# Optimization experiments

Hardware: AMD Instinct MI355X
Metric: run time of the kernel (lower is better)

## Reference

```python
import jax, jax.numpy as jnp
import numpy as np

H = 16          # num_heads
W = 256         # attention_window
D_MODEL = 1024
D_FF = 4096
EPS = 1e-5


def _layernorm(x, g, b):
    mu = jnp.mean(x, axis=-1, keepdims=True)
    var = jnp.mean(jnp.square(x - mu), axis=-1, keepdims=True)
    return (x - mu) * jax.lax.rsqrt(var + EPS) * g + b


def _sliding_attn(q, k, v, w):
    # q,k,v: [B,H,S,d]; each query attends to keys in [i-w, i+w]
    B, Hh, S, d = q.shape
    nc = S // w
    qc = q.reshape(B, Hh, nc, w, d)
    kp = jnp.pad(k, ((0, 0), (0, 0), (w, w), (0, 0)))
    vp = jnp.pad(v, ((0, 0), (0, 0), (w, w), (0, 0)))
    # gather 3w keys per chunk (prev w, current w, next w)
    idx = (jnp.arange(nc) * w)[:, None] + jnp.arange(3 * w)[None, :]  # [nc, 3w]
    kc = kp[:, :, idx, :]  # [B,H,nc,3w,d]
    vc = vp[:, :, idx, :]
    scores = jnp.einsum('bhcqd,bhckd->bhcqk', qc, kc)  # [B,H,nc,w,3w]
    q_pos = jnp.arange(nc)[:, None, None] * w + jnp.arange(w)[None, :, None]
    k_pos = jnp.arange(nc)[:, None, None] * w - w + jnp.arange(3 * w)[None, None, :]
    rel = k_pos - q_pos
    valid = (jnp.abs(rel) <= w) & (k_pos >= 0) & (k_pos < S)  # [nc,w,3w]
    scores = jnp.where(valid[None, None], scores, jnp.float32(-1e9))
    p = jax.nn.softmax(scores, axis=-1)
    out = jnp.einsum('bhcqk,bhckd->bhcqd', p, vc)
    return out.reshape(B, Hh, S, d)


def setup_inputs() -> dict:
    key = jax.random.key(0)
    ks = jax.random.split(key, 8)
    B, S = 2, 4096
    src = jax.random.normal(ks[0], (B, S, D_MODEL), dtype=jnp.float32)
    ln1_g = jnp.ones((D_MODEL,), jnp.float32)
    ln1_b = jnp.zeros((D_MODEL,), jnp.float32)
    ln2_g = jnp.ones((D_MODEL,), jnp.float32)
    ln2_b = jnp.zeros((D_MODEL,), jnp.float32)
    W1 = jax.random.normal(ks[1], (D_MODEL, D_FF), jnp.float32) * 0.02
    b1 = jnp.zeros((D_FF,), jnp.float32)
    W2 = jax.random.normal(ks[2], (D_FF, D_MODEL), jnp.float32) * 0.02
    b2 = jnp.zeros((D_MODEL,), jnp.float32)
    return {"src": src, "ln1_g": ln1_g, "ln1_b": ln1_b, "ln2_g": ln2_g,
            "ln2_b": ln2_b, "W1": W1, "b1": b1, "W2": W2, "b2": b2}


def reference(src, ln1_g, ln1_b, ln2_g, ln2_b, W1, b1, W2, b2):
    B, S, _ = src.shape
    d_head = D_MODEL // H
    qkv = src.reshape(B, S, H, d_head).transpose(0, 2, 1, 3)  # [B,H,S,d]
    attn = _sliding_attn(qkv, qkv, qkv, W)
    attn = attn.transpose(0, 2, 1, 3).reshape(B, S, D_MODEL)
    x = _layernorm(src + attn, ln1_g, ln1_b)
    ff = jnp.maximum(x @ W1 + b1, 0.0) @ W2 + b2
    return _layernorm(x + ff, ln2_g, ln2_b)
```

## Files before the change

kernel.cpp:

```cpp
#include <hip/hip_runtime.h>

typedef __bf16 bf16x8 __attribute__((ext_vector_type(8)));
typedef __bf16 bf16x4 __attribute__((ext_vector_type(4)));
typedef float f32x4 __attribute__((ext_vector_type(4)));

#define MFMA16(a, b, c) __builtin_amdgcn_mfma_f32_16x16x32_bf16((a), (b), (c), 0, 0, 0)

__device__ __forceinline__ void gload_lds16(const void* g, void* l) {
  __builtin_amdgcn_global_load_lds(
      (const __attribute__((address_space(1))) unsigned int*)g,
      (__attribute__((address_space(3))) unsigned int*)l, 16, 0, 0);
}

__global__ __launch_bounds__(512, 2) void attn_kernel(const float* __restrict__ src,
                                                      float* __restrict__ attn_out) {
  const int bid = blockIdx.x;
  const int c = bid & 15;
  const int h = (bid >> 4) & 15;
  const int b = bid >> 8;
  const int tid = threadIdx.x;
  const int w = tid >> 6;
  const int lane = tid & 63;
  const int lg = lane >> 4;
  const int l16 = lane & 15;

  __shared__ __bf16 Ks[64][72];
  __shared__ __bf16 Vt[64][72];

  const int q0 = c * 256 + w * 32;

  bf16x8 qf[2][2];
#pragma unroll
  for (int qfi = 0; qfi < 2; ++qfi)
#pragma unroll
    for (int ks = 0; ks < 2; ++ks) {
      const int row = q0 + qfi * 16 + l16;
      const int d0 = ks * 32 + lg * 8;
      const float* p = src + ((size_t)(b * 4096 + row) * 1024) + h * 64 + d0;
      bf16x8 v;
#pragma unroll
      for (int j = 0; j < 8; ++j) v[j] = (__bf16)p[j];
      qf[qfi][ks] = v;
    }

  int krow[4];
#pragma unroll
  for (int kf = 0; kf < 4; ++kf)
    krow[kf] = ((kf >> 1) << 5) + ((l16 >> 2) << 3) + ((kf & 1) << 2) + (l16 & 3);

  const f32x4 z4 = {0.f, 0.f, 0.f, 0.f};
  float m_run[2], l_run[2];
  f32x4 o[2][4];
#pragma unroll
  for (int qfi = 0; qfi < 2; ++qfi) {
    m_run[qfi] = -6.0e8f;
    l_run[qfi] = 0.f;
#pragma unroll
    for (int df = 0; df < 4; ++df) o[qfi][df] = z4;
  }

  const int stage_key = tid >> 3;
  const int stage_d0 = (tid & 7) * 8;

  for (int kt = 0; kt < 12; ++kt) {
    const int kbase = c * 256 - 256 + kt * 64;
    __syncthreads();
    {
      const int kpos = kbase + stage_key;
      bf16x8 kv;
      if (kpos >= 0 && kpos < 4096) {
        const float* p = src + ((size_t)(b * 4096 + kpos) * 1024) + h * 64 + stage_d0;
#pragma unroll
        for (int j = 0; j < 8; ++j) kv[j] = (__bf16)p[j];
      } else {
#pragma unroll
        for (int j = 0; j < 8; ++j) kv[j] = (__bf16)0.f;
      }
      *(bf16x8*)&Ks[stage_key][stage_d0] = kv;
#pragma unroll
      for (int j = 0; j < 8; ++j) Vt[stage_d0 + j][stage_key] = kv[j];
    }
    __syncthreads();

    const bool skip = (kbase + 63 < 0) | (kbase >= 4096) |
                      (kbase + 63 < q0 - 256) | (kbase > q0 + 31 + 256);
    if (skip) continue;

    f32x4 s[4][2];
#pragma unroll
    for (int kf = 0; kf < 4; ++kf)
#pragma unroll
      for (int qfi = 0; qfi < 2; ++qfi) s[kf][qfi] = z4;

#pragma unroll
    for (int ks = 0; ks < 2; ++ks) {
      bf16x8 ka[4];
#pragma unroll
      for (int kf = 0; kf < 4; ++kf)
        ka[kf] = *(const bf16x8*)&Ks[krow[kf]][ks * 32 + lg * 8];
#pragma unroll
      for (int kf = 0; kf < 4; ++kf)
#pragma unroll
        for (int qfi = 0; qfi < 2; ++qfi)
          s[kf][qfi] = MFMA16(ka[kf], qf[qfi][ks], s[kf][qfi]);
    }

#pragma unroll
    for (int qfi = 0; qfi < 2; ++qfi) {
      const int qp = q0 + qfi * 16 + l16;
#pragma unroll
      for (int kf = 0; kf < 4; ++kf) {
        const int kb0 = kbase + ((kf >> 1) << 5) + 8 * lg + ((kf & 1) << 2);
#pragma unroll
        for (int reg = 0; reg < 4; ++reg) {
          const int kp = kb0 + reg;
          const int rel = kp - qp;
          if (rel > 256 || rel < -256 || kp < 0 || kp >= 4096) s[kf][qfi][reg] = -1e9f;
        }
      }
    }

    bf16x4 pb[4][2];
#pragma unroll
    for (int qfi = 0; qfi < 2; ++qfi) {
      float tm = s[0][qfi][0];
#pragma unroll
      for (int kf = 0; kf < 4; ++kf)
#pragma unroll
        for (int reg = 0; reg < 4; ++reg) tm = fmaxf(tm, s[kf][qfi][reg]);
      tm = fmaxf(tm, __shfl_xor(tm, 16, 64));
      tm = fmaxf(tm, __shfl_xor(tm, 32, 64));

      const float mn = fmaxf(m_run[qfi], tm);
      const float scl = __expf(m_run[qfi] - mn);
      m_run[qfi] = mn;

      float rs = 0.f;
#pragma unroll
      for (int kf = 0; kf < 4; ++kf) {
        bf16x4 pv;
#pragma unroll
        for (int reg = 0; reg < 4; ++reg) {
          const float p = __expf(s[kf][qfi][reg] - mn);
          rs += p;
          pv[reg] = (__bf16)p;
        }
        pb[kf][qfi] = pv;
      }
      rs += __shfl_xor(rs, 16, 64);
      rs += __shfl_xor(rs, 32, 64);
      l_run[qfi] = l_run[qfi] * scl + rs;

#pragma unroll
      for (int df = 0; df < 4; ++df)
#pragma unroll
        for (int reg = 0; reg < 4; ++reg) o[qfi][df][reg] *= scl;
    }

#pragma unroll
    for (int ks2 = 0; ks2 < 2; ++ks2) {
      bf16x8 av[4];
#pragma unroll
      for (int df = 0; df < 4; ++df)
        av[df] = *(const bf16x8*)&Vt[df * 16 + l16][ks2 * 32 + lg * 8];
#pragma unroll
      for (int qfi = 0; qfi < 2; ++qfi) {
        const bf16x8 bq = __builtin_shufflevector(pb[2 * ks2][qfi], pb[2 * ks2 + 1][qfi],
                                                  0, 1, 2, 3, 4, 5, 6, 7);
#pragma unroll
        for (int df = 0; df < 4; ++df)
          o[qfi][df] = MFMA16(av[df], bq, o[qfi][df]);
      }
    }
  }

#pragma unroll
  for (int qfi = 0; qfi < 2; ++qfi) {
    const float inv = 1.0f / l_run[qfi];
    const int qp = q0 + qfi * 16 + l16;
    float* dst = attn_out + ((size_t)(b * 4096 + qp)) * 1024 + h * 64 + lg * 4;
#pragma unroll
    for (int df = 0; df < 4; ++df) {
      float4 r;
      r.x = o[qfi][df][0] * inv;
      r.y = o[qfi][df][1] * inv;
      r.z = o[qfi][df][2] * inv;
      r.w = o[qfi][df][3] * inv;
      *(float4*)&dst[df * 16] = r;
    }
  }
}

template <int MODE>
__global__ __launch_bounds__(512, 2) void gemm8p(const __bf16* __restrict__ A,
                                                 const __bf16* __restrict__ Bt,
                                                 const float* __restrict__ bias,
                                                 void* __restrict__ out0,
                                                 void* __restrict__ out1,
                                                 int M, int N, int Kstride, int Klen) {
  __shared__ char smem[131072];
  const int tid = threadIdx.x;
  const int w = tid >> 6;
  const int lane = tid & 63;
  const int lg = lane >> 4;
  const int l16 = lane & 15;
  const int wr = w >> 2;
  const int wc = w & 3;

  const int nbn = N >> 8;
  const int x = ((int)blockIdx.x & 7) * ((int)gridDim.x >> 3) + ((int)blockIdx.x >> 3);
  const long bm = (long)(x / nbn) * 256;
  const long bn = (long)(x % nbn) * 256;
  const long koff = (long)blockIdx.y * Klen;
  void* out = blockIdx.y ? out1 : out0;

  const f32x4 z4 = {0.f, 0.f, 0.f, 0.f};
  f32x4 acc[8][4];
#pragma unroll
  for (int i = 0; i < 8; ++i)
#pragma unroll
    for (int j = 0; j < 4; ++j) acc[i][j] = z4;

  const int srow = tid >> 2;
  const int g0 = (tid & 3) ^ ((tid >> 3) & 3);
  const __bf16* Ag = A + (size_t)(bm + srow) * Kstride + koff + g0 * 8;
  const __bf16* Bg = Bt + (size_t)(bn + srow) * Kstride + koff + g0 * 8;

  auto stage = [&](int kt, int osel, int isB, int khalf) {
    const __bf16* src = (isB ? Bg : Ag) + (size_t)kt * 64 + khalf * 32;
    char* dst = smem + (isB ? 65536 : 0) + osel * 32768 + khalf * 16384 + (w << 10);
    gload_lds16(src, dst);
    gload_lds16(src + (size_t)128 * Kstride, dst + 8192);
  };

  const int lslot = (lg ^ ((l16 >> 1) & 3)) << 4;
  const char* pA = smem + (wr * 128 + l16) * 64 + lslot;
  const char* pB = smem + 65536 + (wc * 64 + l16) * 64 + lslot;
  auto rdA = [&](int sel, int rf, int ks) {
    return *(const bf16x8*)(pA + sel * 32768 + ks * 16384 + rf * 1024);
  };
  auto rdB = [&](int sel, int cf, int ks) {
    return *(const bf16x8*)(pB + sel * 32768 + ks * 16384 + cf * 1024);
  };

  const int NT = Klen >> 6;

  stage(0, 0, 0, 0);
  stage(0, 0, 1, 0);
  stage(0, 0, 0, 1);
  stage(0, 0, 1, 1);
  asm volatile("s_waitcnt vmcnt(4)" ::: "memory");
  __builtin_amdgcn_s_barrier();

  for (int t = 0; t < NT; ++t) {
    const int sel = t & 1, osel = sel ^ 1;
    const bool st = (t + 1) < NT;
    const int kt1 = t + 1;
    bf16x8 af[8], b0, b1;

#pragma unroll
    for (int rf = 0; rf < 8; ++rf) af[rf] = rdA(sel, rf, 0);
    b0 = rdB(sel, 0, 0);
    b1 = rdB(sel, 1, 0);
    if (st) stage(kt1, osel, 0, 0);
    __builtin_amdgcn_s_barrier();
    asm volatile("s_waitcnt lgkmcnt(0)" ::: "memory");
    __builtin_amdgcn_s_setprio(1);
#pragma unroll
    for (int rf = 0; rf < 8; ++rf) {
      acc[rf][0] = MFMA16(af[rf], b0, acc[rf][0]);
      acc[rf][1] = MFMA16(af[rf], b1, acc[rf][1]);
    }
    __builtin_amdgcn_s_setprio(0);
    __builtin_amdgcn_s_barrier();

    b0 = rdB(sel, 2, 0);
    b1 = rdB(sel, 3, 0);
    if (st) stage(kt1, osel, 1, 0);
    __builtin_amdgcn_s_barrier();
    asm volatile("s_waitcnt lgkmcnt(0)" ::: "memory");
    __builtin_amdgcn_s_setprio(1);
#pragma unroll
    for (int rf = 0; rf < 8; ++rf) {
      acc[rf][2] = MFMA16(af[rf], b0, acc[rf][2]);
      acc[rf][3] = MFMA16(af[rf], b1, acc[rf][3]);
    }
    __builtin_amdgcn_s_setprio(0);
    if (st) asm volatile("s_waitcnt vmcnt(4)" ::: "memory");
    else    asm volatile("s_waitcnt vmcnt(0)" ::: "memory");
    __builtin_amdgcn_s_barrier();

#pragma unroll
    for (int rf = 0; rf < 8; ++rf) af[rf] = rdA(sel, rf, 1);
    b0 = rdB(sel, 0, 1);
    b1 = rdB(sel, 1, 1);
    if (st) stage(kt1, osel, 0, 1);
    __builtin_amdgcn_s_barrier();
    asm volatile("s_waitcnt lgkmcnt(0)" ::: "memory");
    __builtin_amdgcn_s_setprio(1);
#pragma unroll
    for (int rf = 0; rf < 8; ++rf) {
      acc[rf][0] = MFMA16(af[rf], b0, acc[rf][0]);
      acc[rf][1] = MFMA16(af[rf], b1, acc[rf][1]);
    }
    __builtin_amdgcn_s_setprio(0);
    __builtin_amdgcn_s_barrier();

    b0 = rdB(sel, 2, 1);
    b1 = rdB(sel, 3, 1);
    if (st) stage(kt1, osel, 1, 1);
    __builtin_amdgcn_s_barrier();
    asm volatile("s_waitcnt lgkmcnt(0)" ::: "memory");
    __builtin_amdgcn_s_setprio(1);
#pragma unroll
    for (int rf = 0; rf < 8; ++rf) {
      acc[rf][2] = MFMA16(af[rf], b0, acc[rf][2]);
      acc[rf][3] = MFMA16(af[rf], b1, acc[rf][3]);
    }
    __builtin_amdgcn_s_setprio(0);
    if (st) asm volatile("s_waitcnt vmcnt(4)" ::: "memory");
    __builtin_amdgcn_s_barrier();
  }

  float bv[4];
  if (MODE == 0) {
#pragma unroll
    for (int cf = 0; cf < 4; ++cf) bv[cf] = bias[bn + wc * 64 + cf * 16 + l16];
  }
#pragma unroll
  for (int rf = 0; rf < 8; ++rf)
#pragma unroll
    for (int reg = 0; reg < 4; ++reg) {
      const long row = bm + wr * 128 + rf * 16 + lg * 4 + reg;
#pragma unroll
      for (int cf = 0; cf < 4; ++cf) {
        const long col = bn + wc * 64 + cf * 16 + l16;
        if (MODE == 0) {
          const float v = fmaxf(acc[rf][cf][reg] + bv[cf], 0.f);
          ((__bf16*)out)[row * N + col] = (__bf16)v;
        } else {
          ((float*)out)[row * N + col] = acc[rf][cf][reg];
        }
      }
    }
}

__global__ __launch_bounds__(256) void transpose_cvt(const float* __restrict__ in,
                                                     __bf16* __restrict__ out,
                                                     int R, int C) {
  __shared__ float tile[64][65];
  const long r0 = (long)blockIdx.y * 64;
  const long c0 = (long)blockIdx.x * 64;
  const int t = threadIdx.x;
  const int tr = t >> 6;
  const int tc = t & 63;
#pragma unroll
  for (int i = 0; i < 16; ++i) {
    const int r = tr * 16 + i;
    tile[r][tc] = in[(r0 + r) * C + c0 + tc];
  }
  __syncthreads();
#pragma unroll
  for (int i = 0; i < 16; ++i) {
    const int cc = tr * 16 + i;
    out[(c0 + cc) * (long)R + r0 + tc] = (__bf16)tile[tc][cc];
  }
}

__global__ __launch_bounds__(256) void ln1_kernel(const float* __restrict__ src,
                                                  const float* __restrict__ attn,
                                                  const float* __restrict__ g,
                                                  const float* __restrict__ bta,
                                                  __bf16* __restrict__ xb) {
  const long r = blockIdx.x;
  const int t = threadIdx.x;
  const float4 a = *(const float4*)&src[r * 1024 + t * 4];
  const float4 cc = *(const float4*)&attn[r * 1024 + t * 4];
  float v[4] = {a.x + cc.x, a.y + cc.y, a.z + cc.z, a.w + cc.w};
  float s = v[0] + v[1] + v[2] + v[3];
  float s2 = v[0] * v[0] + v[1] * v[1] + v[2] * v[2] + v[3] * v[3];
#pragma unroll
  for (int off = 32; off >= 1; off >>= 1) {
    s += __shfl_xor(s, off, 64);
    s2 += __shfl_xor(s2, off, 64);
  }
  __shared__ float red[8];
  if ((t & 63) == 0) { red[t >> 6] = s; red[(t >> 6) + 4] = s2; }
  __syncthreads();
  s = red[0] + red[1] + red[2] + red[3];
  s2 = red[4] + red[5] + red[6] + red[7];
  const float mu = s * (1.f / 1024.f);
  const float var = s2 * (1.f / 1024.f) - mu * mu;
  const float rstd = rsqrtf(var + 1e-5f);
  const float4 gv = *(const float4*)&g[t * 4];
  const float4 bv = *(const float4*)&bta[t * 4];
  bf16x4 y;
  y[0] = (__bf16)((v[0] - mu) * rstd * gv.x + bv.x);
  y[1] = (__bf16)((v[1] - mu) * rstd * gv.y + bv.y);
  y[2] = (__bf16)((v[2] - mu) * rstd * gv.z + bv.z);
  y[3] = (__bf16)((v[3] - mu) * rstd * gv.w + bv.w);
  *(bf16x4*)&xb[r * 1024 + t * 4] = y;
}

__global__ __launch_bounds__(256) void ln2_kernel(const __bf16* __restrict__ xb,
                                                  const float* __restrict__ f0,
                                                  const float* __restrict__ f1,
                                                  const float* __restrict__ b2,
                                                  const float* __restrict__ g,
                                                  const float* __restrict__ bta,
                                                  float* __restrict__ out) {
  const long r = blockIdx.x;
  const int t = threadIdx.x;
  const bf16x4 xv = *(const bf16x4*)&xb[r * 1024 + t * 4];
  const float4 f0v = *(const float4*)&f0[r * 1024 + t * 4];
  const float4 f1v = *(const float4*)&f1[r * 1024 + t * 4];
  const float4 b2v = *(const float4*)&b2[t * 4];
  float v[4] = {(float)xv[0] + f0v.x + f1v.x + b2v.x,
                (float)xv[1] + f0v.y + f1v.y + b2v.y,
                (float)xv[2] + f0v.z + f1v.z + b2v.z,
                (float)xv[3] + f0v.w + f1v.w + b2v.w};
  float s = v[0] + v[1] + v[2] + v[3];
  float s2 = v[0] * v[0] + v[1] * v[1] + v[2] * v[2] + v[3] * v[3];
#pragma unroll
  for (int off = 32; off >= 1; off >>= 1) {
    s += __shfl_xor(s, off, 64);
    s2 += __shfl_xor(s2, off, 64);
  }
  __shared__ float red[8];
  if ((t & 63) == 0) { red[t >> 6] = s; red[(t >> 6) + 4] = s2; }
  __syncthreads();
  s = red[0] + red[1] + red[2] + red[3];
  s2 = red[4] + red[5] + red[6] + red[7];
  const float mu = s * (1.f / 1024.f);
  const float var = s2 * (1.f / 1024.f) - mu * mu;
  const float rstd = rsqrtf(var + 1e-5f);
  const float4 gv = *(const float4*)&g[t * 4];
  const float4 bv = *(const float4*)&bta[t * 4];
  float4 y;
  y.x = (v[0] - mu) * rstd * gv.x + bv.x;
  y.y = (v[1] - mu) * rstd * gv.y + bv.y;
  y.z = (v[2] - mu) * rstd * gv.z + bv.z;
  y.w = (v[3] - mu) * rstd * gv.w + bv.w;
  *(float4*)&out[r * 1024 + t * 4] = y;
}

extern "C" void kernel_launch(void* const* d_in, const int* in_sizes, int n_in,
                              void* d_out, int out_size, void* d_ws, size_t ws_size,
                              hipStream_t stream) {
  const float* src = (const float*)d_in[0];
  const float* ln1_g = (const float*)d_in[1];
  const float* ln1_b = (const float*)d_in[2];
  const float* ln2_g = (const float*)d_in[3];
  const float* ln2_b = (const float*)d_in[4];
  const float* W1 = (const float*)d_in[5];
  const float* b1 = (const float*)d_in[6];
  const float* W2 = (const float*)d_in[7];
  const float* b2 = (const float*)d_in[8];
  float* out = (float*)d_out;
  char* ws = (char*)d_ws;

  const size_t MB = 1048576;
  float* ff0 = (float*)ws;
  float* ff1 = (float*)(ws + 32 * MB);
  __bf16* xb = (__bf16*)(ws + 64 * MB);
  __bf16* w1t = (__bf16*)(ws + 80 * MB);
  __bf16* w2t = (__bf16*)(ws + 88 * MB);
  __bf16* hbuf = (__bf16*)(ws + 96 * MB);

  int Mc = 8192;
  while (Mc > 512 && 96 * MB + (size_t)Mc * 8192 > ws_size) Mc >>= 1;

  transpose_cvt<<<dim3(4096 / 64, 1024 / 64), 256, 0, stream>>>(W1, w1t, 1024, 4096);
  transpose_cvt<<<dim3(1024 / 64, 4096 / 64), 256, 0, stream>>>(W2, w2t, 4096, 1024);
  attn_kernel<<<512, 512, 0, stream>>>(src, ff0);
  ln1_kernel<<<8192, 256, 0, stream>>>(src, ff0, ln1_g, ln1_b, xb);
  for (int m0 = 0; m0 < 8192; m0 += Mc) {
    gemm8p<0><<<dim3((Mc / 256) * (4096 / 256), 1), 512, 0, stream>>>(
        xb + (size_t)m0 * 1024, w1t, b1, hbuf, hbuf, Mc, 4096, 1024, 1024);
    gemm8p<1><<<dim3((Mc / 256) * (1024 / 256), 2), 512, 0, stream>>>(
        hbuf, w2t, nullptr, ff0 + (size_t)m0 * 1024, ff1 + (size_t)m0 * 1024,
        Mc, 1024, 4096, 2048);
  }
  ln2_kernel<<<8192, 256, 0, stream>>>(xb, ff0, ff1, b2, ln2_g, ln2_b, out);
}
```

Baseline: 256.2 us.

## Prefetch K tiles, swizzle Vt, skip interior masks, exp2 softmax, fewer GEMM barriers

The attention kernel now loads the next key tile into registers while the current tile is being processed, using vectorized float4 loads. It XOR-swizzles the transposed V tile in shared memory to reduce bank conflicts, and skips the window mask on tiles that lie fully inside the window. Softmax uses exp2 with Q pre-scaled by log2(e). The GEMM main loop is cut from four barrier-separated sub-phases per half-step to one, issuing all B-fragment reads and both stage loads together. This lowers synchronisation overhead at the cost of more live registers and a changed ordering between LDS reads and the next stage's writes.

```diff
diff --git a/kernel.cpp b/kernel.cpp
--- a/kernel.cpp
+++ b/kernel.cpp
@@ -23,11 +23,13 @@
   const int lane = tid & 63;
   const int lg = lane >> 4;
   const int l16 = lane & 15;
+  const size_t b4096 = (size_t)b * 4096;
 
   __shared__ __bf16 Ks[64][72];
   __shared__ __bf16 Vt[64][72];
 
   const int q0 = c * 256 + w * 32;
+  const float LOG2E = 1.44269504f;
 
   bf16x8 qf[2][2];
 #pragma unroll
@@ -36,10 +38,10 @@
     for (int ks = 0; ks < 2; ++ks) {
       const int row = q0 + qfi * 16 + l16;
       const int d0 = ks * 32 + lg * 8;
-      const float* p = src + ((size_t)(b * 4096 + row) * 1024) + h * 64 + d0;
+      const float* p = src + (b4096 + row) * 1024 + h * 64 + d0;
       bf16x8 v;
 #pragma unroll
-      for (int j = 0; j < 8; ++j) v[j] = (__bf16)p[j];
+      for (int j = 0; j < 8; ++j) v[j] = (__bf16)(p[j] * LOG2E);
       qf[qfi][ks] = v;
     }
 
@@ -61,26 +63,41 @@
 
   const int stage_key = tid >> 3;
   const int stage_d0 = (tid & 7) * 8;
+  const int vcol = stage_key ^ stage_d0;
+
+  int kpos = c * 256 - 256 + stage_key;
+  float4 ga, gb;
+  {
+    const int rc = min(max(kpos, 0), 4095);
+    const float* p = src + (b4096 + rc) * 1024 + h * 64 + stage_d0;
+    ga = *(const float4*)p;
+    gb = *(const float4*)(p + 4);
+  }
 
   for (int kt = 0; kt < 12; ++kt) {
     const int kbase = c * 256 - 256 + kt * 64;
+    bf16x8 kv;
+    const bool inb = ((unsigned)kpos < 4096u);
+    kv[0] = (__bf16)(inb ? ga.x : 0.f); kv[1] = (__bf16)(inb ? ga.y : 0.f);
+    kv[2] = (__bf16)(inb ? ga.z : 0.f); kv[3] = (__bf16)(inb ? ga.w : 0.f);
+    kv[4] = (__bf16)(inb ? gb.x : 0.f); kv[5] = (__bf16)(inb ? gb.y : 0.f);
+    kv[6] = (__bf16)(inb ? gb.z : 0.f); kv[7] = (__bf16)(inb ? gb.w : 0.f);
+
     __syncthreads();
-    {
-      const int kpos = kbase + stage_key;
-      bf16x8 kv;
-      if (kpos >= 0 && kpos < 4096) {
-        const float* p = src + ((size_t)(b * 4096 + kpos) * 1024) + h * 64 + stage_d0;
-#pragma unroll
-        for (int j = 0; j < 8; ++j) kv[j] = (__bf16)p[j];
-      } else {
-#pragma unroll
-        for (int j = 0; j < 8; ++j) kv[j] = (__bf16)0.f;
-      }
-      *(bf16x8*)&Ks[stage_key][stage_d0] = kv;
-#pragma unroll
-      for (int j = 0; j < 8; ++j) Vt[stage_d0 + j][stage_key] = kv[j];
-    }
-    __syncthreads();
+    *(bf16x8*)&Ks[stage_key][stage_d0] = kv;
+#pragma unroll
+    for (int j = 0; j < 8; ++j) Vt[stage_d0 + j][vcol] = kv[j];
+    asm volatile("s_waitcnt lgkmcnt(0)" ::: "memory");
+    __builtin_amdgcn_s_barrier();
+    __builtin_amdgcn_sched_barrier(0);
+
+    kpos += 64;
+    if (kt < 11) {
+      const int rc = min(max(kpos, 0), 4095);
+      const float* p = src + (b4096 + rc) * 1024 + h * 64 + stage_d0;
+      ga = *(const float4*)p;
+      gb = *(const float4*)(p + 4);
+    }
 
     const bool skip = (kbase + 63 < 0) | (kbase >= 4096) |
                       (kbase + 63 < q0 - 256) | (kbase > q0 + 31 + 256);
@@ -105,17 +122,22 @@
           s[kf][qfi] = MFMA16(ka[kf], qf[qfi][ks], s[kf][qfi]);
     }
 
-#pragma unroll
-    for (int qfi = 0; qfi < 2; ++qfi) {
-      const int qp = q0 + qfi * 16 + l16;
-#pragma unroll
-      for (int kf = 0; kf < 4; ++kf) {
-        const int kb0 = kbase + ((kf >> 1) << 5) + 8 * lg + ((kf & 1) << 2);
-#pragma unroll
-        for (int reg = 0; reg < 4; ++reg) {
-          const int kp = kb0 + reg;
-          const int rel = kp - qp;
-          if (rel > 256 || rel < -256 || kp < 0 || kp >= 4096) s[kf][qfi][reg] = -1e9f;
+    const bool needmask = (kbase < 0) | (kbase > 4032) |
+                          (kbase < q0 - 225) | (kbase > q0 + 193);
+    if (needmask) {
+#pragma unroll
+      for (int qfi = 0; qfi < 2; ++qfi) {
+        const int qp = q0 + qfi * 16 + l16;
+#pragma unroll
+        for (int kf = 0; kf < 4; ++kf) {
+          const int kb0 = kbase + ((kf >> 1) << 5) + 8 * lg + ((kf & 1) << 2);
+#pragma unroll
+          for (int reg = 0; reg < 4; ++reg) {
+            const int kp = kb0 + reg;
+            const int rel = kp - qp;
+            if (rel > 256 || rel < -256 || kp < 0 || kp >= 4096)
+              s[kf][qfi][reg] = -1e9f;
+          }
         }
       }
     }
@@ -132,7 +154,7 @@
       tm = fmaxf(tm, __shfl_xor(tm, 32, 64));
 
       const float mn = fmaxf(m_run[qfi], tm);
-      const float scl = __expf(m_run[qfi] - mn);
+      const float scl = exp2f(m_run[qfi] - mn);
       m_run[qfi] = mn;
 
       float rs = 0.f;
@@ -141,7 +163,7 @@
         bf16x4 pv;
 #pragma unroll
         for (int reg = 0; reg < 4; ++reg) {
-          const float p = __expf(s[kf][qfi][reg] - mn);
+          const float p = exp2f(s[kf][qfi][reg] - mn);
           rs += p;
           pv[reg] = (__bf16)p;
         }
@@ -161,8 +183,11 @@
     for (int ks2 = 0; ks2 < 2; ++ks2) {
       bf16x8 av[4];
 #pragma unroll
-      for (int df = 0; df < 4; ++df)
-        av[df] = *(const bf16x8*)&Vt[df * 16 + l16][ks2 * 32 + lg * 8];
+      for (int df = 0; df < 4; ++df) {
+        const int d = df * 16 + l16;
+        const int blk = (ks2 * 4 + lg) ^ (d >> 3);
+        av[df] = *(const bf16x8*)&Vt[d][blk * 8];
+      }
 #pragma unroll
       for (int qfi = 0; qfi < 2; ++qfi) {
         const bf16x8 bq = __builtin_shufflevector(pb[2 * ks2][qfi], pb[2 * ks2 + 1][qfi],
@@ -178,7 +203,7 @@
   for (int qfi = 0; qfi < 2; ++qfi) {
     const float inv = 1.0f / l_run[qfi];
     const int qp = q0 + qfi * 16 + l16;
-    float* dst = attn_out + ((size_t)(b * 4096 + qp)) * 1024 + h * 64 + lg * 4;
+    float* dst = attn_out + (b4096 + qp) * 1024 + h * 64 + lg * 4;
 #pragma unroll
     for (int df = 0; df < 4; ++df) {
       float4 r;
@@ -251,75 +276,45 @@
   stage(0, 0, 1, 1);
   asm volatile("s_waitcnt vmcnt(4)" ::: "memory");
   __builtin_amdgcn_s_barrier();
+  __builtin_amdgcn_sched_barrier(0);
 
   for (int t = 0; t < NT; ++t) {
     const int sel = t & 1, osel = sel ^ 1;
     const bool st = (t + 1) < NT;
-    const int kt1 = t + 1;
-    bf16x8 af[8], b0, b1;
+    bf16x8 af[8], bf[4];
 
 #pragma unroll
     for (int rf = 0; rf < 8; ++rf) af[rf] = rdA(sel, rf, 0);
-    b0 = rdB(sel, 0, 0);
-    b1 = rdB(sel, 1, 0);
-    if (st) stage(kt1, osel, 0, 0);
-    __builtin_amdgcn_s_barrier();
-    asm volatile("s_waitcnt lgkmcnt(0)" ::: "memory");
+#pragma unroll
+    for (int cf = 0; cf < 4; ++cf) bf[cf] = rdB(sel, cf, 0);
+    if (st) { stage(t + 1, osel, 0, 0); stage(t + 1, osel, 1, 0); }
     __builtin_amdgcn_s_setprio(1);
 #pragma unroll
-    for (int rf = 0; rf < 8; ++rf) {
-      acc[rf][0] = MFMA16(af[rf], b0, acc[rf][0]);
-      acc[rf][1] = MFMA16(af[rf], b1, acc[rf][1]);
-    }
-    __builtin_amdgcn_s_setprio(0);
-    __builtin_amdgcn_s_barrier();
-
-    b0 = rdB(sel, 2, 0);
-    b1 = rdB(sel, 3, 0);
-    if (st) stage(kt1, osel, 1, 0);
-    __builtin_amdgcn_s_barrier();
-    asm volatile("s_waitcnt lgkmcnt(0)" ::: "memory");
-    __builtin_amdgcn_s_setprio(1);
-#pragma unroll
-    for (int rf = 0; rf < 8; ++rf) {
-      acc[rf][2] = MFMA16(af[rf], b0, acc[rf][2]);
-      acc[rf][3] = MFMA16(af[rf], b1, acc[rf][3]);
-    }
+    for (int rf = 0; rf < 8; ++rf)
+#pragma unroll
+      for (int cf = 0; cf < 4; ++cf)
+        acc[rf][cf] = MFMA16(af[rf], bf[cf], acc[rf][cf]);
     __builtin_amdgcn_s_setprio(0);
     if (st) asm volatile("s_waitcnt vmcnt(4)" ::: "memory");
     else    asm volatile("s_waitcnt vmcnt(0)" ::: "memory");
     __builtin_amdgcn_s_barrier();
+    __builtin_amdgcn_sched_barrier(0);
 
 #pragma unroll
     for (int rf = 0; rf < 8; ++rf) af[rf] = rdA(sel, rf, 1);
-    b0 = rdB(sel, 0, 1);
-    b1 = rdB(sel, 1, 1);
-    if (st) stage(kt1, osel, 0, 1);
-    __builtin_amdgcn_s_barrier();
-    asm volatile("s_waitcnt lgkmcnt(0)" ::: "memory");
+#pragma unroll
+    for (int cf = 0; cf < 4; ++cf) bf[cf] = rdB(sel, cf, 1);
+    if (st) { stage(t + 1, osel, 0, 1); stage(t + 1, osel, 1, 1); }
     __builtin_amdgcn_s_setprio(1);
 #pragma unroll
-    for (int rf = 0; rf < 8; ++rf) {
-      acc[rf][0] = MFMA16(af[rf], b0, acc[rf][0]);
-      acc[rf][1] = MFMA16(af[rf], b1, acc[rf][1]);
-    }
-    __builtin_amdgcn_s_setprio(0);
-    __builtin_amdgcn_s_barrier();
-
-    b0 = rdB(sel, 2, 1);
-    b1 = rdB(sel, 3, 1);
-    if (st) stage(kt1, osel, 1, 1);
-    __builtin_amdgcn_s_barrier();
-    asm volatile("s_waitcnt lgkmcnt(0)" ::: "memory");
-    __builtin_amdgcn_s_setprio(1);
-#pragma unroll
-    for (int rf = 0; rf < 8; ++rf) {
-      acc[rf][2] = MFMA16(af[rf], b0, acc[rf][2]);
-      acc[rf][3] = MFMA16(af[rf], b1, acc[rf][3]);
-    }
+    for (int rf = 0; rf < 8; ++rf)
+#pragma unroll
+      for (int cf = 0; cf < 4; ++cf)
+        acc[rf][cf] = MFMA16(af[rf], bf[cf], acc[rf][cf]);
     __builtin_amdgcn_s_setprio(0);
     if (st) asm volatile("s_waitcnt vmcnt(4)" ::: "memory");
     __builtin_amdgcn_s_barrier();
+    __builtin_amdgcn_sched_barrier(0);
   }
 
   float bv[4];
```

After: 253.3 us. About the same (-1.1%).
